# Kernel optimization log

Hardware: AMD Instinct MI355X
Metric: run time of the kernel (lower is better)

Reference implementation:

```python
import jax, jax.numpy as jnp
import numpy as np

B, OUT_LEN, IN_LEN, H = 8, 1024, 4096, 256


def setup_inputs() -> dict:
    key = jax.random.key(0)
    k1, k2, k3 = jax.random.split(key, 3)
    output = jax.random.normal(k1, (B, OUT_LEN, H), dtype=jnp.float32)
    encoder_outputs = jax.random.normal(k2, (B, IN_LEN, H), dtype=jnp.float32)
    # valid lengths in [1, IN_LEN] so every softmax row has >=1 unmasked entry
    lengths = jax.random.randint(k3, (B,), 1, IN_LEN + 1).astype(jnp.int32)
    return {"output": output, "encoder_outputs": encoder_outputs, "lengths": lengths}


def reference(output, encoder_outputs, lengths):
    # scores: [B, out_len, in_len], unscaled dot-product (as in the original)
    scores = jnp.einsum('boh,bih->boi', output, encoder_outputs)
    # mask[b, j] = j < lengths[b]; masked positions get -inf (additive mask)
    valid = jnp.arange(encoder_outputs.shape[1])[None, :] < lengths[:, None]  # [B, in_len]
    scores = jnp.where(valid[:, None, :], scores, -jnp.inf)
    attn = jax.nn.softmax(scores, axis=-1)  # [B, out_len, in_len]
    context = jnp.einsum('boi,bih->boh', attn, encoder_outputs)  # [B, out_len, H]
    return (context, attn)
```

## Files before the change

### kernel.cpp

```cpp
#include <hip/hip_runtime.h>
#include <hip/hip_bf16.h>
#include <math.h>

#define B_    8
#define OLEN  1024
#define ILEN  4096
#define HDIM  256
#define LDA   40

typedef __attribute__((ext_vector_type(8))) short bf16x8;
typedef __attribute__((ext_vector_type(4))) float f32x4;

__device__ inline unsigned pk_bf16(float x, float y) {
  union { __hip_bfloat162 h; unsigned u; } c;
  c.h = __float22bfloat162_rn(make_float2(x, y));
  return c.u;
}
__device__ inline short f2bf(float x) {
  union { __hip_bfloat16 h; short s; } c;
  c.h = __float2bfloat16(x);
  return c.s;
}

struct HiLo { uint4 hi, lo; };
__device__ inline HiLo split8(const float* __restrict__ p) {
  float4 v0 = *(const float4*)p;
  float4 v1 = *(const float4*)(p + 4);
  float f[8] = {v0.x, v0.y, v0.z, v0.w, v1.x, v1.y, v1.z, v1.w};
  unsigned hu[8]; float lo[8];
#pragma unroll
  for (int i = 0; i < 8; ++i) {
    unsigned u = __float_as_uint(f[i]);
    hu[i] = u & 0xffff0000u;
    lo[i] = f[i] - __uint_as_float(hu[i]);
  }
  HiLo r;
  r.hi = make_uint4((hu[0] >> 16) | hu[1], (hu[2] >> 16) | hu[3],
                    (hu[4] >> 16) | hu[5], (hu[6] >> 16) | hu[7]);
  r.lo = make_uint4(pk_bf16(lo[0], lo[1]), pk_bf16(lo[2], lo[3]),
                    pk_bf16(lo[4], lo[5]), pk_bf16(lo[6], lo[7]));
  return r;
}

__device__ inline void gl_lds16(const void* g, void* l) {
  __builtin_amdgcn_global_load_lds(
      (const __attribute__((address_space(1))) unsigned*)g,
      (__attribute__((address_space(3))) unsigned*)(l), 16, 0, 0);
}

__global__ __launch_bounds__(256) void k_prep_q(const float* __restrict__ Q,
                                                short* __restrict__ Qhi,
                                                short* __restrict__ Qlo) {
  const size_t idx = ((size_t)blockIdx.x * 256 + threadIdx.x) * 8;
  HiLo r = split8(&Q[idx]);
  *(uint4*)&Qhi[idx] = r.hi;
  *(uint4*)&Qlo[idx] = r.lo;
}

__global__ __launch_bounds__(256) void k_prep_e(const float* __restrict__ E,
                                                short* __restrict__ Ehi,
                                                short* __restrict__ Elo,
                                                short* __restrict__ ET) {
  const int it = blockIdx.x, ht = blockIdx.y, b = blockIdx.z;
  __shared__ short L[32][36];
  const int t = threadIdx.x;
  {
    const int i = t >> 3, h0 = (t & 7) * 4;
    const size_t gidx = ((size_t)(b * ILEN + it * 32 + i)) * HDIM + ht * 32 + h0;
    float4 v = *(const float4*)&E[gidx];
    float f[4] = {v.x, v.y, v.z, v.w};
    unsigned hs[4]; float lo[4];
#pragma unroll
    for (int j = 0; j < 4; ++j) {
      unsigned u = __float_as_uint(f[j]);
      hs[j] = u & 0xffff0000u;
      lo[j] = f[j] - __uint_as_float(hs[j]);
    }
    *(uint2*)&Ehi[gidx] = make_uint2((hs[0] >> 16) | hs[1], (hs[2] >> 16) | hs[3]);
    *(uint2*)&Elo[gidx] = make_uint2(pk_bf16(lo[0], lo[1]), pk_bf16(lo[2], lo[3]));
    L[h0 + 0][i] = f2bf(f[0]);
    L[h0 + 1][i] = f2bf(f[1]);
    L[h0 + 2][i] = f2bf(f[2]);
    L[h0 + 3][i] = f2bf(f[3]);
  }
  __syncthreads();
  {
    const int h = t >> 3, i0 = (t & 7) * 4;
    *(uint2*)&ET[((size_t)(b * HDIM + ht * 32 + h)) * ILEN + it * 32 + i0] =
        *(const uint2*)&L[h][i0];
  }
}

__global__ __launch_bounds__(256) void k_scores_pre(
    const short* __restrict__ Qhi, const short* __restrict__ Qlo,
    const short* __restrict__ Ehi, const short* __restrict__ Elo,
    float* __restrict__ S) {
  const int it = blockIdx.x, ot = blockIdx.y, b = blockIdx.z;
  const size_t qoff = ((size_t)b * OLEN + ot * 128) * HDIM;
  const size_t eoff = ((size_t)b * ILEN + it * 128) * HDIM;

  __shared__ __align__(16) short Ah[128 * 32], Al[128 * 32];
  __shared__ __align__(16) short Bh[128 * 32], Bl[128 * 32];

  const int t = threadIdx.x;
  const int w = t >> 6, l = t & 63;
  const int la = l & 15, quad = l >> 4;
  const int mw = (w & 1) * 64, nw = (w >> 1) * 64;

  int sgoff[2], sloff[2];
#pragma unroll
  for (int j = 0; j < 2; ++j) {
    const int row = (w * 2 + j) * 16 + (l >> 2);
    const int c = (l & 3) ^ ((row >> 1) & 3);
    sgoff[j] = row * HDIM + c * 8;
    sloff[j] = ((w * 2 + j) * 64 + l) * 8;
  }

  f32x4 acc[4][4] = {};

  for (int kc = 0; kc < HDIM; kc += 32) {
#pragma unroll
    for (int j = 0; j < 2; ++j) {
      const size_t ga = qoff + sgoff[j] + kc;
      const size_t gb = eoff + sgoff[j] + kc;
      gl_lds16(&Qhi[ga], &Ah[sloff[j]]);
      gl_lds16(&Qlo[ga], &Al[sloff[j]]);
      gl_lds16(&Ehi[gb], &Bh[sloff[j]]);
      gl_lds16(&Elo[gb], &Bl[sloff[j]]);
    }
    __syncthreads();
    bf16x8 ah[4], al[4];
#pragma unroll
    for (int mi = 0; mi < 4; ++mi) {
      const int row = mw + mi * 16 + la;
      const int off = row * 32 + (quad ^ ((row >> 1) & 3)) * 8;
      ah[mi] = *(const bf16x8*)&Ah[off];
      al[mi] = *(const bf16x8*)&Al[off];
    }
#pragma unroll
    for (int ni = 0; ni < 4; ++ni) {
      const int row = nw + ni * 16 + la;
      const int off = row * 32 + (quad ^ ((row >> 1) & 3)) * 8;
      bf16x8 bh = *(const bf16x8*)&Bh[off];
      bf16x8 bl = *(const bf16x8*)&Bl[off];
#pragma unroll
      for (int mi = 0; mi < 4; ++mi) {
        acc[mi][ni] = __builtin_amdgcn_mfma_f32_16x16x32_bf16(ah[mi], bh, acc[mi][ni], 0, 0, 0);
        acc[mi][ni] = __builtin_amdgcn_mfma_f32_16x16x32_bf16(ah[mi], bl, acc[mi][ni], 0, 0, 0);
        acc[mi][ni] = __builtin_amdgcn_mfma_f32_16x16x32_bf16(al[mi], bh, acc[mi][ni], 0, 0, 0);
      }
    }
    __syncthreads();
  }

  float* Sb = S + ((size_t)b * OLEN + ot * 128) * (size_t)ILEN + it * 128;
#pragma unroll
  for (int mi = 0; mi < 4; ++mi)
#pragma unroll
    for (int ni = 0; ni < 4; ++ni)
#pragma unroll
      for (int r = 0; r < 4; ++r)
        Sb[(size_t)(mw + mi * 16 + quad * 4 + r) * ILEN + nw + ni * 16 + la] =
            acc[mi][ni][r];
}

__global__ __launch_bounds__(256) void k_softmax(float* __restrict__ A,
                                                 const int* __restrict__ len) {
  const int row = blockIdx.x;
  const int b   = row >> 10;
  const int L   = len[b];
  float* p = A + (size_t)row * ILEN;
  const int t = threadIdx.x;

  float v[16];
#pragma unroll
  for (int k = 0; k < 4; ++k) {
    float4 x = *(const float4*)&p[4 * t + 1024 * k];
    v[4 * k + 0] = x.x; v[4 * k + 1] = x.y;
    v[4 * k + 2] = x.z; v[4 * k + 3] = x.w;
  }
  float m = -INFINITY;
#pragma unroll
  for (int k = 0; k < 4; ++k)
#pragma unroll
    for (int j = 0; j < 4; ++j) {
      const int i = 4 * t + 1024 * k + j;
      if (i < L) m = fmaxf(m, v[4 * k + j]);
    }
  for (int o = 32; o > 0; o >>= 1) m = fmaxf(m, __shfl_xor(m, o, 64));
  __shared__ float sm[4], ss[4];
  const int w = t >> 6;
  if ((t & 63) == 0) sm[w] = m;
  __syncthreads();
  m = fmaxf(fmaxf(sm[0], sm[1]), fmaxf(sm[2], sm[3]));
  float s = 0.f;
#pragma unroll
  for (int k = 0; k < 4; ++k)
#pragma unroll
    for (int j = 0; j < 4; ++j) {
      const int i = 4 * t + 1024 * k + j;
      float pv = (i < L) ? __expf(v[4 * k + j] - m) : 0.f;
      v[4 * k + j] = pv;
      s += pv;
    }
  for (int o = 32; o > 0; o >>= 1) s += __shfl_xor(s, o, 64);
  if ((t & 63) == 0) ss[w] = s;
  __syncthreads();
  s = ss[0] + ss[1] + ss[2] + ss[3];
  const float inv = 1.f / s;
#pragma unroll
  for (int k = 0; k < 4; ++k) {
    float4 x = make_float4(v[4 * k + 0] * inv, v[4 * k + 1] * inv,
                           v[4 * k + 2] * inv, v[4 * k + 3] * inv);
    *(float4*)&p[4 * t + 1024 * k] = x;
  }
}

__global__ __launch_bounds__(256) void k_context_v3(const float* __restrict__ P,
                                                    const short* __restrict__ ET,
                                                    float* __restrict__ Cpart) {
  const int ot = blockIdx.x, ks = blockIdx.y, b = blockIdx.z;
  const float* Pb = P + ((size_t)b * OLEN + ot * 64) * (size_t)ILEN + ks * 2048;
  const short* Tb = ET + (size_t)b * HDIM * ILEN + ks * 2048;

  __shared__ __align__(16) short As[64 * 64];
  __shared__ __align__(16) short Bs[256 * 64];

  const int t = threadIdx.x;
  const int w = t >> 6, l = t & 63;
  const int la = l & 15, quad = l >> 4;
  const int mw = (w & 1) * 32, nw = (w >> 1) * 128;

  const int tr = t >> 2, tc = t & 3;
  const int ac0 = tc * 2;
  int bslot[8];
#pragma unroll
  for (int j = 0; j < 8; ++j) bslot[j] = w * 512 + j * 64 + l;

  f32x4 acc[2][8] = {};

  for (int ic = 0; ic < 2048; ic += 64) {
#pragma unroll
    for (int j = 0; j < 8; ++j) {
      const int s = bslot[j];
      const int row = s >> 3, pc = s & 7;
      const int c = pc ^ (row & 7);
      gl_lds16(&Tb[(size_t)row * ILEN + ic + c * 8], &Bs[s * 8]);
    }
    {
      const float* src = &Pb[(size_t)tr * ILEN + ic + tc * 16];
      float4 f0 = *(const float4*)src;
      float4 f1 = *(const float4*)(src + 4);
      float4 f2 = *(const float4*)(src + 8);
      float4 f3 = *(const float4*)(src + 12);
      uint4 w0 = make_uint4(pk_bf16(f0.x, f0.y), pk_bf16(f0.z, f0.w),
                            pk_bf16(f1.x, f1.y), pk_bf16(f1.z, f1.w));
      uint4 w1 = make_uint4(pk_bf16(f2.x, f2.y), pk_bf16(f2.z, f2.w),
                            pk_bf16(f3.x, f3.y), pk_bf16(f3.z, f3.w));
      *(uint4*)&As[tr * 64 + ((ac0) ^ (tr & 7)) * 8] = w0;
      *(uint4*)&As[tr * 64 + ((ac0 + 1) ^ (tr & 7)) * 8] = w1;
    }
    __syncthreads();
#pragma unroll
    for (int ki = 0; ki < 2; ++ki) {
      bf16x8 af[2];
#pragma unroll
      for (int mi = 0; mi < 2; ++mi) {
        const int row = mw + mi * 16 + la;
        af[mi] = *(const bf16x8*)&As[row * 64 + ((ki * 4 + quad) ^ (row & 7)) * 8];
      }
#pragma unroll
      for (int ni = 0; ni < 8; ++ni) {
        const int row = nw + ni * 16 + la;
        bf16x8 bfr = *(const bf16x8*)&Bs[row * 64 + ((ki * 4 + quad) ^ (row & 7)) * 8];
#pragma unroll
        for (int mi = 0; mi < 2; ++mi)
          acc[mi][ni] = __builtin_amdgcn_mfma_f32_16x16x32_bf16(af[mi], bfr,
                                                               acc[mi][ni], 0, 0, 0);
      }
    }
    __syncthreads();
  }

  float* Cb = Cpart + (size_t)ks * (B_ * OLEN * HDIM) +
              ((size_t)b * OLEN + ot * 64) * HDIM;
#pragma unroll
  for (int mi = 0; mi < 2; ++mi)
#pragma unroll
    for (int ni = 0; ni < 8; ++ni)
#pragma unroll
      for (int r = 0; r < 4; ++r)
        Cb[(size_t)(mw + mi * 16 + quad * 4 + r) * HDIM + nw + ni * 16 + la] =
            acc[mi][ni][r];
}

__global__ __launch_bounds__(256) void k_reduce(const float* __restrict__ Cp,
                                                float* __restrict__ ctx) {
  const size_t idx = ((size_t)blockIdx.x * 256 + threadIdx.x) * 8;
  const size_t n = (size_t)B_ * OLEN * HDIM;
  float4 a0 = *(const float4*)&Cp[idx];
  float4 a1 = *(const float4*)&Cp[idx + 4];
  float4 b0 = *(const float4*)&Cp[n + idx];
  float4 b1 = *(const float4*)&Cp[n + idx + 4];
  *(float4*)&ctx[idx] = make_float4(a0.x + b0.x, a0.y + b0.y, a0.z + b0.z, a0.w + b0.w);
  *(float4*)&ctx[idx + 4] = make_float4(a1.x + b1.x, a1.y + b1.y, a1.z + b1.z, a1.w + b1.w);
}

__global__ __launch_bounds__(256) void k_etrans(const float* __restrict__ E,
                                                short* __restrict__ ET) {
  const int it = blockIdx.x, ht = blockIdx.y, b = blockIdx.z;
  __shared__ short L[32][36];
  const int t = threadIdx.x;
  {
    const int i = t >> 3, h0 = (t & 7) * 4;
    float4 v = *(const float4*)&E[((size_t)(b * ILEN + it * 32 + i)) * HDIM + ht * 32 + h0];
    L[h0 + 0][i] = f2bf(v.x);
    L[h0 + 1][i] = f2bf(v.y);
    L[h0 + 2][i] = f2bf(v.z);
    L[h0 + 3][i] = f2bf(v.w);
  }
  __syncthreads();
  {
    const int h = t >> 3, i0 = (t & 7) * 4;
    *(uint2*)&ET[((size_t)(b * HDIM + ht * 32 + h)) * ILEN + it * 32 + i0] =
        *(const uint2*)&L[h][i0];
  }
}

__global__ __launch_bounds__(256) void k_scores_split(const float* __restrict__ Q,
                                                      const float* __restrict__ E,
                                                      float* __restrict__ S) {
  const int b = blockIdx.z, ot = blockIdx.y, it = blockIdx.x;
  const float* Qb = Q + ((size_t)b * OLEN + ot * 64) * HDIM;
  const float* Eb = E + ((size_t)b * ILEN + it * 64) * HDIM;

  __shared__ __align__(16) short Ah[64 * LDA], Al[64 * LDA];
  __shared__ __align__(16) short Bh[64 * LDA], Bl[64 * LDA];

  const int t = threadIdx.x;
  const int w = t >> 6, l = t & 63;
  const int la = l & 15, quad = l >> 4;
  const int sr = t >> 2, sc = (t & 3) * 8;

  f32x4 acc[4] = {};

#pragma unroll
  for (int kc = 0; kc < HDIM; kc += 32) {
    HiLo qa = split8(&Qb[(size_t)sr * HDIM + kc + sc]);
    HiLo eb = split8(&Eb[(size_t)sr * HDIM + kc + sc]);
    *(uint4*)&Ah[sr * LDA + sc] = qa.hi;
    *(uint4*)&Al[sr * LDA + sc] = qa.lo;
    *(uint4*)&Bh[sr * LDA + sc] = eb.hi;
    *(uint4*)&Bl[sr * LDA + sc] = eb.lo;
    __syncthreads();
    bf16x8 ah = *(const bf16x8*)&Ah[(w * 16 + la) * LDA + quad * 8];
    bf16x8 al = *(const bf16x8*)&Al[(w * 16 + la) * LDA + quad * 8];
#pragma unroll
    for (int n = 0; n < 4; ++n) {
      bf16x8 bh = *(const bf16x8*)&Bh[(n * 16 + la) * LDA + quad * 8];
      bf16x8 bl = *(const bf16x8*)&Bl[(n * 16 + la) * LDA + quad * 8];
      acc[n] = __builtin_amdgcn_mfma_f32_16x16x32_bf16(ah, bh, acc[n], 0, 0, 0);
      acc[n] = __builtin_amdgcn_mfma_f32_16x16x32_bf16(ah, bl, acc[n], 0, 0, 0);
      acc[n] = __builtin_amdgcn_mfma_f32_16x16x32_bf16(al, bh, acc[n], 0, 0, 0);
    }
    __syncthreads();
  }

  float* Sb = S + ((size_t)b * OLEN + ot * 64) * (size_t)ILEN + it * 64;
#pragma unroll
  for (int n = 0; n < 4; ++n)
#pragma unroll
    for (int r = 0; r < 4; ++r)
      Sb[(size_t)(w * 16 + quad * 4 + r) * ILEN + n * 16 + la] = acc[n][r];
}

__global__ __launch_bounds__(256) void k_context_f32(const float* __restrict__ P,
                                                     const short* __restrict__ ET,
                                                     float* __restrict__ C) {
  const int ot = blockIdx.x, ht = blockIdx.y, b = blockIdx.z;
  const float* Pb = P + ((size_t)b * OLEN + ot * 64) * (size_t)ILEN;
  const short* Tb = ET + ((size_t)b * HDIM + ht * 64) * (size_t)ILEN;

  __shared__ __align__(16) short As[64 * LDA], Bs[64 * LDA];

  const int t = threadIdx.x;
  const int w = t >> 6, l = t & 63;
  const int la = l & 15, quad = l >> 4;
  const int sr = t >> 2, sc = (t & 3) * 8;

  f32x4 acc[4] = {};

  for (int ic = 0; ic < ILEN; ic += 32) {
    {
      float4 p0 = *(const float4*)&Pb[(size_t)sr * ILEN + ic + sc];
      float4 p1 = *(const float4*)&Pb[(size_t)sr * ILEN + ic + sc + 4];
      uint4 aw = make_uint4(pk_bf16(p0.x, p0.y), pk_bf16(p0.z, p0.w),
                            pk_bf16(p1.x, p1.y), pk_bf16(p1.z, p1.w));
      *(uint4*)&As[sr * LDA + sc] = aw;
      uint4 bw = *(const uint4*)&Tb[(size_t)sr * ILEN + ic + sc];
      *(uint4*)&Bs[sr * LDA + sc] = bw;
    }
    __syncthreads();
    bf16x8 a = *(const bf16x8*)&As[(w * 16 + la) * LDA + quad * 8];
#pragma unroll
    for (int n = 0; n < 4; ++n) {
      bf16x8 bb = *(const bf16x8*)&Bs[(n * 16 + la) * LDA + quad * 8];
      acc[n] = __builtin_amdgcn_mfma_f32_16x16x32_bf16(a, bb, acc[n], 0, 0, 0);
    }
    __syncthreads();
  }

  float* Cb = C + ((size_t)b * OLEN + ot * 64) * HDIM + ht * 64;
#pragma unroll
  for (int n = 0; n < 4; ++n)
#pragma unroll
    for (int r = 0; r < 4; ++r)
      Cb[(size_t)(w * 16 + quad * 4 + r) * HDIM + n * 16 + la] = acc[n][r];
}

extern "C" void kernel_launch(void* const* d_in, const int* in_sizes, int n_in,
                              void* d_out, int out_size, void* d_ws, size_t ws_size,
                              hipStream_t stream) {
  (void)in_sizes; (void)n_in; (void)out_size;
  const float* outp = (const float*)d_in[0];
  const float* enc  = (const float*)d_in[1];
  const int*   len  = (const int*)d_in[2];

  float* ctx  = (float*)d_out;
  float* attn = ctx + (size_t)B_ * OLEN * HDIM;

  short* ws = (short*)d_ws;
  const size_t M = 1024 * 1024;
  short* ET = ws;

  if (ws_size >= 56ull * 1024 * 1024) {
    short* Qhi = ws + 8 * M;
    short* Qlo = ws + 10 * M;
    short* Ehi = ws + 12 * M;
    short* Elo = ws + 20 * M;
    float* Cpart = (float*)(ws + 8 * M);
    k_prep_q<<<(B_ * OLEN * HDIM) / (256 * 8), 256, 0, stream>>>(outp, Qhi, Qlo);
    dim3 gp(ILEN / 32, HDIM / 32, B_);
    k_prep_e<<<gp, 256, 0, stream>>>(enc, Ehi, Elo, ET);
    dim3 g1(ILEN / 128, OLEN / 128, B_);
    k_scores_pre<<<g1, 256, 0, stream>>>(Qhi, Qlo, Ehi, Elo, attn);
    k_softmax<<<B_ * OLEN, 256, 0, stream>>>(attn, len);
    dim3 g3(OLEN / 64, 2, B_);
    k_context_v3<<<g3, 256, 0, stream>>>(attn, ET, Cpart);
    k_reduce<<<(B_ * OLEN * HDIM) / (256 * 8), 256, 0, stream>>>(Cpart, ctx);
  } else {
    dim3 gt(ILEN / 32, HDIM / 32, B_);
    k_etrans<<<gt, 256, 0, stream>>>(enc, ET);
    k_scores_split<<<dim3(ILEN / 64, OLEN / 64, B_), 256, 0, stream>>>(outp, enc, attn);
    k_softmax<<<B_ * OLEN, 256, 0, stream>>>(attn, len);
    dim3 g3(OLEN / 64, HDIM / 64, B_);
    k_context_f32<<<g3, 256, 0, stream>>>(attn, ET, ctx);
  }
}
```

Baseline: 321.6 us.

## Fuse softmax into scores and context kernels with length-based tile skipping

Removes the standalone softmax pass. The scores kernel now emits per-tile row max and sum, a small combine kernel merges them into per-row max and inverse sum, and the context kernel applies exp and normalisation on the fly while writing the final attention. Tiles beyond each batch's valid length are skipped in the scores, prep and context kernels, and masked attention regions are zero-filled directly. This saves a full read/write round trip over the attention matrix plus the masked GEMM work, in exchange for extra exp work in the context loop and scratch stats stored in the ctx output buffer.

```diff
diff --git a/kernel.cpp b/kernel.cpp
--- a/kernel.cpp
+++ b/kernel.cpp
@@ -60,10 +60,18 @@
 __global__ __launch_bounds__(256) void k_prep_e(const float* __restrict__ E,
                                                 short* __restrict__ Ehi,
                                                 short* __restrict__ Elo,
-                                                short* __restrict__ ET) {
+                                                short* __restrict__ ET,
+                                                const int* __restrict__ len) {
   const int it = blockIdx.x, ht = blockIdx.y, b = blockIdx.z;
-  __shared__ short L[32][36];
-  const int t = threadIdx.x;
+  const int L = len[b];
+  const int t = threadIdx.x;
+  if (it * 32 >= L) {
+    const int h = t >> 3, i0 = (t & 7) * 4;
+    *(uint2*)&ET[((size_t)(b * HDIM + ht * 32 + h)) * ILEN + it * 32 + i0] =
+        make_uint2(0u, 0u);
+    return;
+  }
+  __shared__ short Lsh[32][36];
   {
     const int i = t >> 3, h0 = (t & 7) * 4;
     const size_t gidx = ((size_t)(b * ILEN + it * 32 + i)) * HDIM + ht * 32 + h0;
@@ -78,24 +86,28 @@
     }
     *(uint2*)&Ehi[gidx] = make_uint2((hs[0] >> 16) | hs[1], (hs[2] >> 16) | hs[3]);
     *(uint2*)&Elo[gidx] = make_uint2(pk_bf16(lo[0], lo[1]), pk_bf16(lo[2], lo[3]));
-    L[h0 + 0][i] = f2bf(f[0]);
-    L[h0 + 1][i] = f2bf(f[1]);
-    L[h0 + 2][i] = f2bf(f[2]);
-    L[h0 + 3][i] = f2bf(f[3]);
+    Lsh[h0 + 0][i] = f2bf(f[0]);
+    Lsh[h0 + 1][i] = f2bf(f[1]);
+    Lsh[h0 + 2][i] = f2bf(f[2]);
+    Lsh[h0 + 3][i] = f2bf(f[3]);
   }
   __syncthreads();
   {
     const int h = t >> 3, i0 = (t & 7) * 4;
     *(uint2*)&ET[((size_t)(b * HDIM + ht * 32 + h)) * ILEN + it * 32 + i0] =
-        *(const uint2*)&L[h][i0];
+        *(const uint2*)&Lsh[h][i0];
   }
 }
 
 __global__ __launch_bounds__(256) void k_scores_pre(
     const short* __restrict__ Qhi, const short* __restrict__ Qlo,
     const short* __restrict__ Ehi, const short* __restrict__ Elo,
-    float* __restrict__ S) {
+    float* __restrict__ S, float2* __restrict__ stat,
+    const int* __restrict__ len) {
   const int it = blockIdx.x, ot = blockIdx.y, b = blockIdx.z;
+  const int L = len[b];
+  if (it * 128 >= L) return;
+
   const size_t qoff = ((size_t)b * OLEN + ot * 128) * HDIM;
   const size_t eoff = ((size_t)b * ILEN + it * 128) * HDIM;
 
@@ -162,66 +174,101 @@
       for (int r = 0; r < 4; ++r)
         Sb[(size_t)(mw + mi * 16 + quad * 4 + r) * ILEN + nw + ni * 16 + la] =
             acc[mi][ni][r];
-}
-
-__global__ __launch_bounds__(256) void k_softmax(float* __restrict__ A,
+
+  float* SM = (float*)Ah;
+  float* SS = SM + 256;
+  const int colbase = it * 128 + nw;
+
+  float rmax[4][4];
+#pragma unroll
+  for (int mi = 0; mi < 4; ++mi)
+#pragma unroll
+    for (int r = 0; r < 4; ++r) {
+      float mx = -INFINITY;
+#pragma unroll
+      for (int ni = 0; ni < 4; ++ni)
+        if (colbase + ni * 16 + la < L) mx = fmaxf(mx, acc[mi][ni][r]);
+      rmax[mi][r] = mx;
+    }
+#pragma unroll
+  for (int o = 1; o < 16; o <<= 1)
+#pragma unroll
+    for (int mi = 0; mi < 4; ++mi)
+#pragma unroll
+      for (int r = 0; r < 4; ++r)
+        rmax[mi][r] = fmaxf(rmax[mi][r], __shfl_xor(rmax[mi][r], o, 64));
+  if (la == 0) {
+#pragma unroll
+    for (int mi = 0; mi < 4; ++mi)
+#pragma unroll
+      for (int r = 0; r < 4; ++r)
+        SM[(w >> 1) * 128 + mw + mi * 16 + quad * 4 + r] = rmax[mi][r];
+  }
+  __syncthreads();
+
+  float rsum[4][4];
+#pragma unroll
+  for (int mi = 0; mi < 4; ++mi)
+#pragma unroll
+    for (int r = 0; r < 4; ++r) {
+      const int row = mw + mi * 16 + quad * 4 + r;
+      const float M = fmaxf(SM[row], SM[128 + row]);
+      float s = 0.f;
+#pragma unroll
+      for (int ni = 0; ni < 4; ++ni)
+        if (colbase + ni * 16 + la < L) s += __expf(acc[mi][ni][r] - M);
+      rsum[mi][r] = s;
+    }
+#pragma unroll
+  for (int o = 1; o < 16; o <<= 1)
+#pragma unroll
+    for (int mi = 0; mi < 4; ++mi)
+#pragma unroll
+      for (int r = 0; r < 4; ++r)
+        rsum[mi][r] += __shfl_xor(rsum[mi][r], o, 64);
+  if (la == 0) {
+#pragma unroll
+    for (int mi = 0; mi < 4; ++mi)
+#pragma unroll
+      for (int r = 0; r < 4; ++r)
+        SS[(w >> 1) * 128 + mw + mi * 16 + quad * 4 + r] = rsum[mi][r];
+  }
+  __syncthreads();
+
+  if (t < 128) {
+    const float m = fmaxf(SM[t], SM[128 + t]);
+    const float s = SS[t] + SS[128 + t];
+    stat[(size_t)it * (B_ * OLEN) + (size_t)b * OLEN + ot * 128 + t] =
+        make_float2(m, s);
+  }
+}
+
+__global__ __launch_bounds__(256) void k_combine(const float2* __restrict__ stat,
+                                                 float2* __restrict__ rowstat,
                                                  const int* __restrict__ len) {
-  const int row = blockIdx.x;
-  const int b   = row >> 10;
-  const int L   = len[b];
-  float* p = A + (size_t)row * ILEN;
-  const int t = threadIdx.x;
-
-  float v[16];
-#pragma unroll
-  for (int k = 0; k < 4; ++k) {
-    float4 x = *(const float4*)&p[4 * t + 1024 * k];
-    v[4 * k + 0] = x.x; v[4 * k + 1] = x.y;
-    v[4 * k + 2] = x.z; v[4 * k + 3] = x.w;
-  }
+  const int row = blockIdx.x * 256 + threadIdx.x;
+  const int b = row >> 10;
+  const int L = len[b];
+  const int nt = (L + 127) >> 7;
   float m = -INFINITY;
-#pragma unroll
-  for (int k = 0; k < 4; ++k)
-#pragma unroll
-    for (int j = 0; j < 4; ++j) {
-      const int i = 4 * t + 1024 * k + j;
-      if (i < L) m = fmaxf(m, v[4 * k + j]);
-    }
-  for (int o = 32; o > 0; o >>= 1) m = fmaxf(m, __shfl_xor(m, o, 64));
-  __shared__ float sm[4], ss[4];
-  const int w = t >> 6;
-  if ((t & 63) == 0) sm[w] = m;
-  __syncthreads();
-  m = fmaxf(fmaxf(sm[0], sm[1]), fmaxf(sm[2], sm[3]));
+  for (int it = 0; it < nt; ++it)
+    m = fmaxf(m, stat[(size_t)it * (B_ * OLEN) + row].x);
   float s = 0.f;
-#pragma unroll
-  for (int k = 0; k < 4; ++k)
-#pragma unroll
-    for (int j = 0; j < 4; ++j) {
-      const int i = 4 * t + 1024 * k + j;
-      float pv = (i < L) ? __expf(v[4 * k + j] - m) : 0.f;
-      v[4 * k + j] = pv;
-      s += pv;
-    }
-  for (int o = 32; o > 0; o >>= 1) s += __shfl_xor(s, o, 64);
-  if ((t & 63) == 0) ss[w] = s;
-  __syncthreads();
-  s = ss[0] + ss[1] + ss[2] + ss[3];
-  const float inv = 1.f / s;
-#pragma unroll
-  for (int k = 0; k < 4; ++k) {
-    float4 x = make_float4(v[4 * k + 0] * inv, v[4 * k + 1] * inv,
-                           v[4 * k + 2] * inv, v[4 * k + 3] * inv);
-    *(float4*)&p[4 * t + 1024 * k] = x;
-  }
-}
-
-__global__ __launch_bounds__(256) void k_context_v3(const float* __restrict__ P,
-                                                    const short* __restrict__ ET,
-                                                    float* __restrict__ Cpart) {
+  for (int it = 0; it < nt; ++it) {
+    float2 v = stat[(size_t)it * (B_ * OLEN) + row];
+    s += v.y * __expf(v.x - m);
+  }
+  rowstat[row] = make_float2(m, 1.f / s);
+}
+
+__global__ __launch_bounds__(256) void k_context_fused(
+    float* __restrict__ P, const short* __restrict__ ET,
+    float* __restrict__ Cpart, const float2* __restrict__ rowstat,
+    const int* __restrict__ len) {
   const int ot = blockIdx.x, ks = blockIdx.y, b = blockIdx.z;
-  const float* Pb = P + ((size_t)b * OLEN + ot * 64) * (size_t)ILEN + ks * 2048;
+  float* Pb = P + ((size_t)b * OLEN + ot * 64) * (size_t)ILEN + ks * 2048;
   const short* Tb = ET + (size_t)b * HDIM * ILEN + ks * 2048;
+  const int L = len[b];
 
   __shared__ __align__(16) short As[64 * 64];
   __shared__ __align__(16) short Bs[256 * 64];
@@ -233,6 +280,9 @@
 
   const int tr = t >> 2, tc = t & 3;
   const int ac0 = tc * 2;
+  const float2 st = rowstat[(size_t)b * OLEN + ot * 64 + tr];
+  const float rm = st.x, rinv = st.y;
+
   int bslot[8];
 #pragma unroll
   for (int j = 0; j < 8; ++j) bslot[j] = w * 512 + j * 64 + l;
@@ -240,6 +290,16 @@
   f32x4 acc[2][8] = {};
 
   for (int ic = 0; ic < 2048; ic += 64) {
+    const int ibase = ks * 2048 + ic;
+    float* arow = &Pb[(size_t)tr * ILEN + ic + tc * 16];
+    if (ibase >= L) {
+      const float4 z = make_float4(0.f, 0.f, 0.f, 0.f);
+      *(float4*)(arow + 0) = z;
+      *(float4*)(arow + 4) = z;
+      *(float4*)(arow + 8) = z;
+      *(float4*)(arow + 12) = z;
+      continue;
+    }
 #pragma unroll
     for (int j = 0; j < 8; ++j) {
       const int s = bslot[j];
@@ -248,15 +308,24 @@
       gl_lds16(&Tb[(size_t)row * ILEN + ic + c * 8], &Bs[s * 8]);
     }
     {
-      const float* src = &Pb[(size_t)tr * ILEN + ic + tc * 16];
-      float4 f0 = *(const float4*)src;
-      float4 f1 = *(const float4*)(src + 4);
-      float4 f2 = *(const float4*)(src + 8);
-      float4 f3 = *(const float4*)(src + 12);
-      uint4 w0 = make_uint4(pk_bf16(f0.x, f0.y), pk_bf16(f0.z, f0.w),
-                            pk_bf16(f1.x, f1.y), pk_bf16(f1.z, f1.w));
-      uint4 w1 = make_uint4(pk_bf16(f2.x, f2.y), pk_bf16(f2.z, f2.w),
-                            pk_bf16(f3.x, f3.y), pk_bf16(f3.z, f3.w));
+      float4 f0 = *(const float4*)(arow + 0);
+      float4 f1 = *(const float4*)(arow + 4);
+      float4 f2 = *(const float4*)(arow + 8);
+      float4 f3 = *(const float4*)(arow + 12);
+      float v[16] = {f0.x, f0.y, f0.z, f0.w, f1.x, f1.y, f1.z, f1.w,
+                     f2.x, f2.y, f2.z, f2.w, f3.x, f3.y, f3.z, f3.w};
+      const int i0 = ibase + tc * 16;
+#pragma unroll
+      for (int j = 0; j < 16; ++j)
+        v[j] = (i0 + j < L) ? __expf(v[j] - rm) * rinv : 0.f;
+      *(float4*)(arow + 0)  = make_float4(v[0], v[1], v[2], v[3]);
+      *(float4*)(arow + 4)  = make_float4(v[4], v[5], v[6], v[7]);
+      *(float4*)(arow + 8)  = make_float4(v[8], v[9], v[10], v[11]);
+      *(float4*)(arow + 12) = make_float4(v[12], v[13], v[14], v[15]);
+      uint4 w0 = make_uint4(pk_bf16(v[0], v[1]), pk_bf16(v[2], v[3]),
+                            pk_bf16(v[4], v[5]), pk_bf16(v[6], v[7]));
+      uint4 w1 = make_uint4(pk_bf16(v[8], v[9]), pk_bf16(v[10], v[11]),
+                            pk_bf16(v[12], v[13]), pk_bf16(v[14], v[15]));
       *(uint4*)&As[tr * 64 + ((ac0) ^ (tr & 7)) * 8] = w0;
       *(uint4*)&As[tr * 64 + ((ac0 + 1) ^ (tr & 7)) * 8] = w1;
     }
@@ -306,24 +375,76 @@
   *(float4*)&ctx[idx + 4] = make_float4(a1.x + b1.x, a1.y + b1.y, a1.z + b1.z, a1.w + b1.w);
 }
 
+__global__ __launch_bounds__(256) void k_softmax(float* __restrict__ A,
+                                                 const int* __restrict__ len) {
+  const int row = blockIdx.x;
+  const int b   = row >> 10;
+  const int L   = len[b];
+  float* p = A + (size_t)row * ILEN;
+  const int t = threadIdx.x;
+
+  float v[16];
+#pragma unroll
+  for (int k = 0; k < 4; ++k) {
+    float4 x = *(const float4*)&p[4 * t + 1024 * k];
+    v[4 * k + 0] = x.x; v[4 * k + 1] = x.y;
+    v[4 * k + 2] = x.z; v[4 * k + 3] = x.w;
+  }
+  float m = -INFINITY;
+#pragma unroll
+  for (int k = 0; k < 4; ++k)
+#pragma unroll
+    for (int j = 0; j < 4; ++j) {
+      const int i = 4 * t + 1024 * k + j;
+      if (i < L) m = fmaxf(m, v[4 * k + j]);
+    }
+  for (int o = 32; o > 0; o >>= 1) m = fmaxf(m, __shfl_xor(m, o, 64));
+  __shared__ float sm[4], ss[4];
+  const int w = t >> 6;
+  if ((t & 63) == 0) sm[w] = m;
+  __syncthreads();
+  m = fmaxf(fmaxf(sm[0], sm[1]), fmaxf(sm[2], sm[3]));
+  float s = 0.f;
+#pragma unroll
+  for (int k = 0; k < 4; ++k)
+#pragma unroll
+    for (int j = 0; j < 4; ++j) {
+      const int i = 4 * t + 1024 * k + j;
+      float pv = (i < L) ? __expf(v[4 * k + j] - m) : 0.f;
+      v[4 * k + j] = pv;
+      s += pv;
+    }
+  for (int o = 32; o > 0; o >>= 1) s += __shfl_xor(s, o, 64);
+  if ((t & 63) == 0) ss[w] = s;
+  __syncthreads();
+  s = ss[0] + ss[1] + ss[2] + ss[3];
+  const float inv = 1.f / s;
+#pragma unroll
+  for (int k = 0; k < 4; ++k) {
+    float4 x = make_float4(v[4 * k + 0] * inv, v[4 * k + 1] * inv,
+                           v[4 * k + 2] * inv, v[4 * k + 3] * inv);
+    *(float4*)&p[4 * t + 1024 * k] = x;
+  }
+}
+
 __global__ __launch_bounds__(256) void k_etrans(const float* __restrict__ E,
                                                 short* __restrict__ ET) {
   const int it = blockIdx.x, ht = blockIdx.y, b = blockIdx.z;
-  __shared__ short L[32][36];
+  __shared__ short Lsh[32][36];
   const int t = threadIdx.x;
   {
     const int i = t >> 3, h0 = (t & 7) * 4;
     float4 v = *(const float4*)&E[((size_t)(b * ILEN + it * 32 + i)) * HDIM + ht * 32 + h0];
-    L[h0 + 0][i] = f2bf(v.x);
-    L[h0 + 1][i] = f2bf(v.y);
-    L[h0 + 2][i] = f2bf(v.z);
-    L[h0 + 3][i] = f2bf(v.w);
+    Lsh[h0 + 0][i] = f2bf(v.x);
+    Lsh[h0 + 1][i] = f2bf(v.y);
+    Lsh[h0 + 2][i] = f2bf(v.z);
+    Lsh[h0 + 3][i] = f2bf(v.w);
   }
   __syncthreads();
   {
     const int h = t >> 3, i0 = (t & 7) * 4;
     *(uint2*)&ET[((size_t)(b * HDIM + ht * 32 + h)) * ILEN + it * 32 + i0] =
-        *(const uint2*)&L[h][i0];
+        *(const uint2*)&Lsh[h][i0];
   }
 }
 
@@ -439,14 +560,17 @@
     short* Ehi = ws + 12 * M;
     short* Elo = ws + 20 * M;
     float* Cpart = (float*)(ws + 8 * M);
+    float2* stat = (float2*)ctx;
+    float2* rowstat = stat + (size_t)(ILEN / 128) * B_ * OLEN;
+
     k_prep_q<<<(B_ * OLEN * HDIM) / (256 * 8), 256, 0, stream>>>(outp, Qhi, Qlo);
     dim3 gp(ILEN / 32, HDIM / 32, B_);
-    k_prep_e<<<gp, 256, 0, stream>>>(enc, Ehi, Elo, ET);
+    k_prep_e<<<gp, 256, 0, stream>>>(enc, Ehi, Elo, ET, len);
     dim3 g1(ILEN / 128, OLEN / 128, B_);
-    k_scores_pre<<<g1, 256, 0, stream>>>(Qhi, Qlo, Ehi, Elo, attn);
-    k_softmax<<<B_ * OLEN, 256, 0, stream>>>(attn, len);
+    k_scores_pre<<<g1, 256, 0, stream>>>(Qhi, Qlo, Ehi, Elo, attn, stat, len);
+    k_combine<<<(B_ * OLEN) / 256, 256, 0, stream>>>(stat, rowstat, len);
     dim3 g3(OLEN / 64, 2, B_);
-    k_context_v3<<<g3, 256, 0, stream>>>(attn, ET, Cpart);
+    k_context_fused<<<g3, 256, 0, stream>>>(attn, ET, Cpart, rowstat, len);
     k_reduce<<<(B_ * OLEN * HDIM) / (256 * 8), 256, 0, stream>>>(Cpart, ctx);
   } else {
     dim3 gt(ILEN / 32, HDIM / 32, B_);
```

Result: no change. 323.1 us (+0.5%).
